# Kernel tuning notes

Measured on AMD Instinct MI355X. Metric: run time of the kernel, lower is better.

The kernel has to match this reference:

```python
import jax, jax.numpy as jnp
import numpy as np

B, T, E, H, L, V = 2, 1024, 1024, 16, 4, 32000
HS = E // H
EPS = 1e-5


def layernorm(x, g, b):
    m = jnp.mean(x, axis=-1, keepdims=True)
    v = jnp.mean((x - m) ** 2, axis=-1, keepdims=True)
    return (x - m) * jax.lax.rsqrt(v + EPS) * g + b


def setup_inputs() -> dict:
    key = jax.random.key(0)
    ks = jax.random.split(key, 20)
    s = 0.02
    inp = {
        "ids": jax.random.randint(ks[0], (B, T), 0, V, dtype=jnp.int32),
        "emb": jax.random.normal(ks[1], (V, E), jnp.float32) * s,
        "pos": jax.random.normal(ks[2], (T, E), jnp.float32) * s,
        "wq": jax.random.normal(ks[3], (L, E, E), jnp.float32) * s,
        "bq": jnp.zeros((L, E), jnp.float32),
        "wk": jax.random.normal(ks[4], (L, E, E), jnp.float32) * s,
        "bk": jnp.zeros((L, E), jnp.float32),
        "wv": jax.random.normal(ks[5], (L, E, E), jnp.float32) * s,
        "bv": jnp.zeros((L, E), jnp.float32),
        "w1": jax.random.normal(ks[6], (L, E, 4 * E), jnp.float32) * s,
        "b1": jnp.zeros((L, 4 * E), jnp.float32),
        "w2": jax.random.normal(ks[7], (L, 4 * E, E), jnp.float32) * s,
        "b2": jnp.zeros((L, E), jnp.float32),
        "ln1_g": jnp.ones((L, E), jnp.float32),
        "ln1_b": jnp.zeros((L, E), jnp.float32),
        "ln2_g": jnp.ones((L, E), jnp.float32),
        "ln2_b": jnp.zeros((L, E), jnp.float32),
        "proj_w": jax.random.normal(ks[8], (E, V), jnp.float32) * s,
        "proj_b": jnp.zeros((V,), jnp.float32),
    }
    return inp


def reference(ids, emb, pos, wq, bq, wk, bk, wv, bv, w1, b1, w2, b2,
              ln1_g, ln1_b, ln2_g, ln2_b, proj_w, proj_b):
    x = emb[ids] + pos[:ids.shape[-1]]  # [B,T,E]
    scale = 1.0 / (E ** 0.5)  # NOTE: original divides by embed_size**0.5
    causal = jnp.tril(jnp.ones((T, T), dtype=bool))
    for l in range(L):
        h = layernorm(x, ln1_g[l], ln1_b[l])
        q = (h @ wq[l] + bq[l]).reshape(B, T, H, HS).transpose(0, 2, 1, 3)
        k = (h @ wk[l] + bk[l]).reshape(B, T, H, HS).transpose(0, 2, 1, 3)
        v = (h @ wv[l] + bv[l]).reshape(B, T, H, HS).transpose(0, 2, 1, 3)
        scores = jnp.einsum('bhqd,bhkd->bhqk', q, k) * scale
        scores = jnp.where(causal, scores, -jnp.inf)
        attn = jax.nn.softmax(scores, axis=-1)
        o = jnp.einsum('bhqk,bhkd->bhqd', attn, v)
        o = o.transpose(0, 2, 1, 3).reshape(B, T, E)
        x = x + o
        h2 = layernorm(x, ln2_g[l], ln2_b[l])
        ff = jax.nn.gelu(h2 @ w1[l] + b1[l], approximate=False) @ w2[l] + b2[l]
        x = x + ff  # Dropout(0.2) in eval mode = identity
    logits = x @ proj_w + proj_b  # [B,T,V]
    return logits
```

## Files before the change

kernel.cpp:

```cpp
#include <hip/hip_runtime.h>
#include <hip/hip_bf16.h>
#include <cstdint>

#define B_    2
#define T_    1024
#define E_    1024
#define H_    16
#define HS_   64
#define L_    4
#define V_    32000
#define FF_   4096
#define BT_   2048
#define EPS_  1e-5f
#define SCALE_ 0.03125f

typedef __bf16 bf16;
typedef bf16  bf16x4 __attribute__((ext_vector_type(4)));
typedef bf16  bf16x8 __attribute__((ext_vector_type(8)));
typedef float f32x4  __attribute__((ext_vector_type(4)));

#define GL2LDS(gp, lp) __builtin_amdgcn_global_load_lds( \
    (const __attribute__((address_space(1))) void*)(gp), \
    (__attribute__((address_space(3))) void*)(lp), 16, 0, 0)

__global__ __launch_bounds__(256) void embed_kernel(
    const int* __restrict__ ids, const float* __restrict__ emb,
    const float* __restrict__ pos, float* __restrict__ x)
{
  int bt = blockIdx.x;
  int t  = bt & (T_ - 1);
  int id = ids[bt];
  f32x4 e = *(const f32x4*)(emb + (size_t)id * E_ + threadIdx.x * 4);
  f32x4 p = *(const f32x4*)(pos + (size_t)t  * E_ + threadIdx.x * 4);
  *(f32x4*)(x + (size_t)bt * E_ + threadIdx.x * 4) = e + p;
}

__device__ __forceinline__ float wred_sum(float v) {
#pragma unroll
  for (int o = 32; o; o >>= 1) v += __shfl_xor(v, o, 64);
  return v;
}

__global__ __launch_bounds__(256) void ln_kernel(
    const float* __restrict__ x, const float* __restrict__ g,
    const float* __restrict__ b, bf16* __restrict__ h)
{
  int row = blockIdx.x, tid = threadIdx.x;
  f32x4 v = *(const f32x4*)(x + (size_t)row * E_ + tid * 4);
  float s  = v[0] + v[1] + v[2] + v[3];
  float sq = v[0]*v[0] + v[1]*v[1] + v[2]*v[2] + v[3]*v[3];
  s  = wred_sum(s);
  sq = wred_sum(sq);
  __shared__ float rs[4], rq[4];
  int w = tid >> 6, lane = tid & 63;
  if (lane == 0) { rs[w] = s; rq[w] = sq; }
  __syncthreads();
  float S = rs[0] + rs[1] + rs[2] + rs[3];
  float Q = rq[0] + rq[1] + rq[2] + rq[3];
  float mean = S * (1.0f / E_);
  float var  = Q * (1.0f / E_) - mean * mean;
  float rstd = rsqrtf(fmaxf(var, 0.0f) + EPS_);
  f32x4 gv = *(const f32x4*)(g + tid * 4);
  f32x4 bv = *(const f32x4*)(b + tid * 4);
  f32x4 o = (v - mean) * rstd * gv + bv;
  bf16x4 ob = { (bf16)o[0], (bf16)o[1], (bf16)o[2], (bf16)o[3] };
  *(bf16x4*)(h + (size_t)row * E_ + tid * 4) = ob;
}

__global__ __launch_bounds__(256) void convw_kernel(
    const float* __restrict__ W0, const float* __restrict__ W1, const float* __restrict__ W2,
    bf16* __restrict__ O0, bf16* __restrict__ O1, bf16* __restrict__ O2,
    int K, int ldW)
{
  int z = blockIdx.z;
  const float* W = (z == 0) ? W0 : (z == 1) ? W1 : W2;
  bf16*        O = (z == 0) ? O0 : (z == 1) ? O1 : O2;
  __shared__ float tl[32][33];
  int n0 = blockIdx.x * 32, k0 = blockIdx.y * 32;
  int c = threadIdx.x & 31, r = threadIdx.x >> 5;
#pragma unroll
  for (int p = 0; p < 4; ++p)
    tl[r + p * 8][c] = W[(size_t)(k0 + r + p * 8) * ldW + n0 + c];
  __syncthreads();
#pragma unroll
  for (int p = 0; p < 4; ++p)
    O[(size_t)(n0 + r + p * 8) * K + k0 + c] = (bf16)tl[c][r + p * 8];
}

template <int ACT, int MODE>
__global__ __launch_bounds__(256) void gemm_bf16(
    const bf16* __restrict__ A,
    const bf16* __restrict__ B0, const bf16* __restrict__ B1, const bf16* __restrict__ B2,
    const float* __restrict__ bi0, const float* __restrict__ bi1, const float* __restrict__ bi2,
    bf16* __restrict__ Cb0, bf16* __restrict__ Cb1, bf16* __restrict__ Cb2,
    float* __restrict__ Cf,
    int K, int ldc, int LDK)
{
  int z = blockIdx.z;
  const bf16*  Bm = (MODE == 3) ? B0 : (z == 0) ? B0 : (z == 1) ? B1 : B2;
  const float* bi = (z == 0) ? bi0 : (z == 1) ? bi1 : bi2;
  bf16*        Cb = (z == 0) ? Cb0 : (z == 1) ? Cb1 : Cb2;
  int koff = (MODE == 3) ? z * K : 0;

  int nb  = (int)(gridDim.x * gridDim.y);
  int lin = blockIdx.x + gridDim.x * blockIdx.y;
  int per = nb >> 3;
  int b   = (lin & 7) * per + (lin >> 3);
  int mi  = b & 15;
  int ni  = b >> 4;

  __shared__ __align__(16) char lds[2][16384];

  int tid = threadIdx.x;
  int lane = tid & 63, wid = tid >> 6;
  int wm = (wid >> 1) * 64, wn = (wid & 1) * 64;
  int fr = lane & 15, fb = lane >> 4;

  const bf16* Asrc = A  + (size_t)(mi * 128) * LDK + koff;
  const bf16* Bsrc = Bm + (size_t)(ni * 128) * LDK + koff;

  int NT = K >> 5;

#define STAGE(buf, kk)                                                          \
  {                                                                             \
    _Pragma("unroll")                                                           \
    for (int is = 0; is < 2; ++is) {                                            \
      int rl = is * 64 + (tid >> 2);                                            \
      int key = (rl >> 1) & 3;                                                  \
      int ck  = ((tid & 3) ^ key) * 8;                                          \
      GL2LDS(Asrc + (size_t)rl * LDK + (kk) + ck,                               \
             lds[buf] + is * 4096 + tid * 16);                                  \
      GL2LDS(Bsrc + (size_t)rl * LDK + (kk) + ck,                               \
             lds[buf] + 8192 + is * 4096 + tid * 16);                           \
    }                                                                           \
  }

  f32x4 acc[4][4];
#pragma unroll
  for (int i = 0; i < 4; ++i)
#pragma unroll
    for (int j = 0; j < 4; ++j) acc[i][j] = (f32x4){0.f, 0.f, 0.f, 0.f};

  STAGE(0, 0);
  int cur = 0;

  for (int t = 0; t < NT; ++t) {
    __syncthreads();
    if (t + 1 < NT) STAGE(cur ^ 1, (t + 1) << 5);

    const char* Ab = lds[cur];
    const char* Bb = lds[cur] + 8192;
    bf16x8 af[4], bfr[4];
#pragma unroll
    for (int i = 0; i < 4; ++i) {
      int rl = wm + i * 16 + fr;
      af[i] = *(const bf16x8*)(Ab + rl * 64 + ((fb ^ ((rl >> 1) & 3)) * 16));
    }
#pragma unroll
    for (int j = 0; j < 4; ++j) {
      int rl = wn + j * 16 + fr;
      bfr[j] = *(const bf16x8*)(Bb + rl * 64 + ((fb ^ ((rl >> 1) & 3)) * 16));
    }
#pragma unroll
    for (int i = 0; i < 4; ++i)
#pragma unroll
      for (int j = 0; j < 4; ++j)
        acc[i][j] = __builtin_amdgcn_mfma_f32_16x16x32_bf16(af[i], bfr[j], acc[i][j], 0, 0, 0);
    cur ^= 1;
  }
#undef STAGE

#pragma unroll
  for (int i = 0; i < 4; ++i) {
#pragma unroll
    for (int j = 0; j < 4; ++j) {
      int gc = ni * 128 + wn + j * 16 + fr;
      float bv = (MODE == 3) ? 0.f : bi[gc];
#pragma unroll
      for (int r = 0; r < 4; ++r) {
        int gr = mi * 128 + wm + i * 16 + fb * 4 + r;
        float vv = acc[i][j][r] + bv;
        if (ACT == 1) vv = 0.5f * vv * (1.0f + erff(vv * 0.70710678118654752f));
        if (MODE == 1) {
          Cb[(size_t)gr * ldc + gc] = (bf16)vv;
        } else {
          Cf[(size_t)(blockIdx.z * BT_ + gr) * ldc + gc] = vv;
        }
      }
    }
  }
}

__global__ __launch_bounds__(256) void combine_kernel(
    const float* __restrict__ p, const float* __restrict__ bi,
    float* __restrict__ x, bf16* __restrict__ xb)
{
  int row = blockIdx.x, tid = threadIdx.x;
  size_t off = (size_t)row * E_ + tid * 4;
  f32x4 a = *(const f32x4*)(p + off);
  f32x4 c = *(const f32x4*)(p + (size_t)BT_ * E_ + off);
  f32x4 bv = *(const f32x4*)(bi + tid * 4);
  f32x4 xv = *(const f32x4*)(x + off);
  f32x4 nv = xv + a + c + bv;
  *(f32x4*)(x + off) = nv;
  bf16x4 ob = { (bf16)nv[0], (bf16)nv[1], (bf16)nv[2], (bf16)nv[3] };
  *(bf16x4*)(xb + off) = ob;
}

__global__ __launch_bounds__(512, 2) void gemm256_kernel(
    const bf16* __restrict__ A, const bf16* __restrict__ Bm,
    const float* __restrict__ bi, float* __restrict__ C, int K, int N)
{
  int nwg = (int)gridDim.x;
  int per = nwg >> 3;
  int bid = (int)blockIdx.x;
  int tl  = (bid & 7) * per + (bid >> 3);
  int mi  = tl & 7, ni = tl >> 3;

  __shared__ __align__(16) char lds[2][65536];

  int tid = threadIdx.x;
  int lane = tid & 63, wid = tid >> 6;
  int wr = wid >> 2, wc = wid & 3;
  int fr = lane & 15, fb = lane >> 4;

  const bf16* Asrc = A  + (size_t)(mi * 256) * K;
  const bf16* Bsrc = Bm + (size_t)(ni * 256) * K;

  int NT = K >> 6;

#define STGQ(buf, kk, h, is)                                               \
  {                                                                        \
    int ri  = (is) * 64 + (tid >> 3);                                      \
    int ck  = (tid & 7) ^ (ri & 7);                                        \
    int row = (h) * 128 + ri;                                              \
    GL2LDS(Asrc + (size_t)row * K + (kk) + ck * 8,                         \
           lds[buf] + (h) * 16384 + (is) * 8192 + tid * 16);               \
    GL2LDS(Bsrc + (size_t)row * K + (kk) + ck * 8,                         \
           lds[buf] + 32768 + (h) * 16384 + (is) * 8192 + tid * 16);       \
  }

  f32x4 acc[8][4];
#pragma unroll
  for (int i = 0; i < 8; ++i)
#pragma unroll
    for (int j = 0; j < 4; ++j) acc[i][j] = (f32x4){0.f, 0.f, 0.f, 0.f};

  STGQ(0, 0, 0, 0); STGQ(0, 0, 0, 1); STGQ(0, 0, 1, 0); STGQ(0, 0, 1, 1);

  for (int t = 0; t < NT; ++t) {
    int buf = t & 1;
    int nk  = (t + 1) << 6;
    bool pf = (t + 1 < NT);

    if (pf) {
      STGQ(buf ^ 1, nk, 0, 0);
      asm volatile("s_waitcnt vmcnt(2)" ::: "memory");
    } else {
      asm volatile("s_waitcnt vmcnt(0)" ::: "memory");
    }
    __builtin_amdgcn_s_barrier();
    asm volatile("" ::: "memory");

    const char* Ab = lds[buf];
    const char* Bb = lds[buf] + 32768;

    bf16x8 bfr[4][2];
#pragma unroll
    for (int n2 = 0; n2 < 4; ++n2) {
      int row = wc * 64 + n2 * 16 + fr;
#pragma unroll
      for (int ks = 0; ks < 2; ++ks)
        bfr[n2][ks] = *(const bf16x8*)(Bb + (row >> 7) * 16384 + (row & 127) * 128
                                          + ((((ks * 4 + fb) ^ (fr & 7))) << 4));
    }

#pragma unroll
    for (int q = 0; q < 4; ++q) {
      bf16x8 af[2][2];
#pragma unroll
      for (int m2 = 0; m2 < 2; ++m2) {
        int ri = (q * 2 + m2) * 16 + fr;
#pragma unroll
        for (int ks = 0; ks < 2; ++ks)
          af[m2][ks] = *(const bf16x8*)(Ab + wr * 16384 + ri * 128
                                           + ((((ks * 4 + fb) ^ (fr & 7))) << 4));
      }
      __builtin_amdgcn_s_setprio(1);
#pragma unroll
      for (int m2 = 0; m2 < 2; ++m2)
#pragma unroll
        for (int n2 = 0; n2 < 4; ++n2)
#pragma unroll
          for (int ks = 0; ks < 2; ++ks)
            acc[q * 2 + m2][n2] = __builtin_amdgcn_mfma_f32_16x16x32_bf16(
                af[m2][ks], bfr[n2][ks], acc[q * 2 + m2][n2], 0, 0, 0);
      __builtin_amdgcn_s_setprio(0);
      if (pf && q == 0) STGQ(buf ^ 1, nk, 0, 1);
      if (pf && q == 1) STGQ(buf ^ 1, nk, 1, 0);
      if (pf && q == 2) STGQ(buf ^ 1, nk, 1, 1);
    }
    asm volatile("" ::: "memory");
    __builtin_amdgcn_s_barrier();
  }
#undef STGQ

#pragma unroll
  for (int i = 0; i < 8; ++i) {
#pragma unroll
    for (int j = 0; j < 4; ++j) {
      int gc = ni * 256 + wc * 64 + j * 16 + fr;
      float bv = bi[gc];
#pragma unroll
      for (int r = 0; r < 4; ++r) {
        int gr = mi * 256 + wr * 128 + i * 16 + fb * 4 + r;
        C[(size_t)gr * N + gc] = acc[i][j][r] + bv;
      }
    }
  }
}

__global__ __launch_bounds__(256) void attn_kernel(
    const bf16* __restrict__ q, const bf16* __restrict__ k,
    const bf16* __restrict__ v, float* __restrict__ x)
{
  __shared__ __align__(16) char Ks[8192];
  __shared__ __align__(16) char Vs[8192];
  __shared__ __align__(16) char Ps[8192];

  int tid = threadIdx.x, lane = tid & 63, w = tid >> 6;
  int qt = blockIdx.x, bh = blockIdx.y;
  int b = bh >> 4, h = bh & 15;
  size_t hoff = (size_t)b * T_ * E_ + h * HS_;
  int fr = lane & 15, fb = lane >> 4;

  bf16x8 qa[2];
  {
    const bf16* qp = q + hoff + (size_t)(qt * 64 + w * 16 + fr) * E_ + fb * 8;
    qa[0] = *(const bf16x8*)qp;
    qa[1] = *(const bf16x8*)(qp + 32);
  }

  f32x4 O[4];
  float m_[4], l_[4];
#pragma unroll
  for (int i = 0; i < 4; ++i) { O[i] = (f32x4){0.f,0.f,0.f,0.f}; m_[i] = -1e30f; l_[i] = 0.f; }

  for (int kt = 0; kt <= qt; ++kt) {
    __syncthreads();
    {
      const bf16* kbase = k + hoff + (size_t)(kt * 64) * E_;
#pragma unroll
      for (int is = 0; is < 2; ++is) {
        int c = is * 32 + (tid >> 3);
        int key = ((c & 7) ^ (c >> 3)) & 7;
        GL2LDS(kbase + (size_t)c * E_ + (((tid & 7) ^ key) * 8),
               Ks + is * 4096 + tid * 16);
      }
    }
#pragma unroll
    for (int p = 0; p < 2; ++p) {
      int row = tid >> 2;
      int d0 = (tid & 3) * 8 + p * 32;
      bf16x8 vv = *(const bf16x8*)(v + hoff + (size_t)(kt * 64 + row) * E_ + d0);
#pragma unroll
      for (int e = 0; e < 8; ++e) {
        int d = d0 + e;
        int key = ((d & 7) ^ (d >> 3)) & 7;
        *(bf16*)(Vs + d * 128 + ((row * 2) ^ (key << 4))) = vv[e];
      }
    }
    __syncthreads();

    f32x4 s[4];
#pragma unroll
    for (int jc = 0; jc < 4; ++jc) {
      s[jc] = (f32x4){0.f, 0.f, 0.f, 0.f};
#pragma unroll
      for (int kc = 0; kc < 2; ++kc) {
        int c = jc * 16 + fr;
        int key = ((c & 7) ^ (c >> 3)) & 7;
        bf16x8 kf = *(const bf16x8*)(Ks + c * 128 + ((kc * 64 + fb * 16) ^ (key << 4)));
        s[jc] = __builtin_amdgcn_mfma_f32_16x16x32_bf16(qa[kc], kf, s[jc], 0, 0, 0);
      }
    }

    char* pbase = Ps + w * 2048;
#pragma unroll
    for (int r = 0; r < 4; ++r) {
      float s0 = s[0][r] * SCALE_, s1 = s[1][r] * SCALE_;
      float s2 = s[2][r] * SCALE_, s3 = s[3][r] * SCALE_;
      int qrow = qt * 64 + w * 16 + fb * 4 + r;
      if (kt == qt) {
        int kc0 = kt * 64 + fr;
        if (kc0      > qrow) s0 = -1e30f;
        if (kc0 + 16 > qrow) s1 = -1e30f;
        if (kc0 + 32 > qrow) s2 = -1e30f;
        if (kc0 + 48 > qrow) s3 = -1e30f;
      }
      float mx = fmaxf(fmaxf(s0, s1), fmaxf(s2, s3));
      mx = fmaxf(mx, __shfl_xor(mx, 1, 16));
      mx = fmaxf(mx, __shfl_xor(mx, 2, 16));
      mx = fmaxf(mx, __shfl_xor(mx, 4, 16));
      mx = fmaxf(mx, __shfl_xor(mx, 8, 16));
      float mnew = fmaxf(m_[r], mx);
      float p0 = __expf(s0 - mnew), p1 = __expf(s1 - mnew);
      float p2 = __expf(s2 - mnew), p3 = __expf(s3 - mnew);
      float rs = p0 + p1 + p2 + p3;
      rs += __shfl_xor(rs, 1, 16);
      rs += __shfl_xor(rs, 2, 16);
      rs += __shfl_xor(rs, 4, 16);
      rs += __shfl_xor(rs, 8, 16);
      float scl = __expf(m_[r] - mnew);
      l_[r] = l_[r] * scl + rs;
      m_[r] = mnew;
#pragma unroll
      for (int jd = 0; jd < 4; ++jd) O[jd][r] *= scl;
      int key2 = (r << 4) ^ (fb << 5);
      char* pr_ = pbase + (fb * 4 + r) * 128;
      *(bf16*)(pr_ + (( 0 + fr * 2) ^ key2)) = (bf16)p0;
      *(bf16*)(pr_ + ((32 + fr * 2) ^ key2)) = (bf16)p1;
      *(bf16*)(pr_ + ((64 + fr * 2) ^ key2)) = (bf16)p2;
      *(bf16*)(pr_ + ((96 + fr * 2) ^ key2)) = (bf16)p3;
    }

#pragma unroll
    for (int kc = 0; kc < 2; ++kc) {
      int key2 = ((fr & 3) << 4) ^ ((fr >> 2) << 5);
      bf16x8 pa = *(const bf16x8*)(pbase + fr * 128 + ((kc * 64 + fb * 16) ^ key2));
#pragma unroll
      for (int jd = 0; jd < 4; ++jd) {
        int d = jd * 16 + fr;
        int key = ((d & 7) ^ (d >> 3)) & 7;
        bf16x8 vf = *(const bf16x8*)(Vs + d * 128 + ((kc * 64 + fb * 16) ^ (key << 4)));
        O[jd] = __builtin_amdgcn_mfma_f32_16x16x32_bf16(pa, vf, O[jd], 0, 0, 0);
      }
    }
  }

#pragma unroll
  for (int r = 0; r < 4; ++r) {
    float inv = 1.0f / l_[r];
    float* xp = x + hoff + (size_t)(qt * 64 + w * 16 + fb * 4 + r) * E_;
#pragma unroll
    for (int jd = 0; jd < 4; ++jd) {
      int d = jd * 16 + fr;
      xp[d] += O[jd][r] * inv;
    }
  }
}

extern "C" void kernel_launch(void* const* d_in, const int* in_sizes, int n_in,
                              void* d_out, int out_size, void* d_ws, size_t ws_size,
                              hipStream_t stream)
{
  const int*   ids  = (const int*)  d_in[0];
  const float* emb  = (const float*)d_in[1];
  const float* pos  = (const float*)d_in[2];
  const float* wq   = (const float*)d_in[3];
  const float* bq   = (const float*)d_in[4];
  const float* wk   = (const float*)d_in[5];
  const float* bk   = (const float*)d_in[6];
  const float* wv   = (const float*)d_in[7];
  const float* bv   = (const float*)d_in[8];
  const float* w1   = (const float*)d_in[9];
  const float* b1   = (const float*)d_in[10];
  const float* w2   = (const float*)d_in[11];
  const float* b2   = (const float*)d_in[12];
  const float* ln1g = (const float*)d_in[13];
  const float* ln1b = (const float*)d_in[14];
  const float* ln2g = (const float*)d_in[15];
  const float* ln2b = (const float*)d_in[16];
  const float* pw   = (const float*)d_in[17];
  const float* pb   = (const float*)d_in[18];
  float* out = (float*)d_out;

  if (ws_size < (size_t)17 * 1024 * 1024 * 4) return;
  float* ws = (float*)d_ws;
  float* x   = ws;
  bf16*  hb  = (bf16*)(ws + (size_t) 2 * 1024 * 1024);
  bf16*  qb  = (bf16*)(ws + (size_t) 3 * 1024 * 1024);
  bf16*  kb  = (bf16*)(ws + (size_t) 4 * 1024 * 1024);
  bf16*  vb  = (bf16*)(ws + (size_t) 5 * 1024 * 1024);
  bf16*  ffb = (bf16*)(ws + (size_t) 6 * 1024 * 1024);
  float* fp  = ws + (size_t)2 * 1024 * 1024;
  bf16*  lwb = (bf16*)(ws + (size_t)10 * 1024 * 1024);
  bf16*  xb  = (bf16*)(ws + (size_t)16 * 1024 * 1024);
  bf16*  pwb = (bf16*)ws;
  bf16*  wqt = lwb;
  bf16*  wkt = lwb + (size_t)1 * 1024 * 1024;
  bf16*  wvt = lwb + (size_t)2 * 1024 * 1024;
  bf16*  w1t = lwb + (size_t)3 * 1024 * 1024;
  bf16*  w2t = lwb + (size_t)7 * 1024 * 1024;

  embed_kernel<<<BT_, 256, 0, stream>>>(ids, emb, pos, x);

  for (int l = 0; l < L_; ++l) {
    const size_t lEE = (size_t)l * E_ * E_;
    const size_t lEF = (size_t)l * E_ * FF_;

    convw_kernel<<<dim3(E_/32, E_/32, 3), 256, 0, stream>>>(
        wq + lEE, wk + lEE, wv + lEE, wqt, wkt, wvt, E_, E_);
    convw_kernel<<<dim3(FF_/32, E_/32, 1), 256, 0, stream>>>(
        w1 + lEF, nullptr, nullptr, w1t, nullptr, nullptr, E_, FF_);
    convw_kernel<<<dim3(E_/32, FF_/32, 1), 256, 0, stream>>>(
        w2 + lEF, nullptr, nullptr, w2t, nullptr, nullptr, FF_, E_);

    ln_kernel<<<BT_, 256, 0, stream>>>(x, ln1g + l*E_, ln1b + l*E_, hb);

    gemm_bf16<0,1><<<dim3(16, E_/128, 3), 256, 0, stream>>>(
        hb, wqt, wkt, wvt, bq + l*E_, bk + l*E_, bv + l*E_,
        qb, kb, vb, nullptr, E_, E_, E_);

    attn_kernel<<<dim3(T_/64, B_*H_), 256, 0, stream>>>(qb, kb, vb, x);

    ln_kernel<<<BT_, 256, 0, stream>>>(x, ln2g + l*E_, ln2b + l*E_, hb);

    gemm_bf16<1,1><<<dim3(16, FF_/128, 1), 256, 0, stream>>>(
        hb, w1t, nullptr, nullptr, b1 + (size_t)l*FF_, nullptr, nullptr,
        ffb, nullptr, nullptr, nullptr, E_, FF_, E_);

    gemm_bf16<0,3><<<dim3(16, E_/128, 2), 256, 0, stream>>>(
        ffb, w2t, nullptr, nullptr, nullptr, nullptr, nullptr,
        nullptr, nullptr, nullptr, fp, FF_/2, E_, FF_);
    combine_kernel<<<BT_, 256, 0, stream>>>(fp, b2 + l*E_, x, xb);
  }

  convw_kernel<<<dim3(V_/32, E_/32, 1), 256, 0, stream>>>(
      pw, nullptr, nullptr, pwb, nullptr, nullptr, E_, V_);
  gemm256_kernel<<<(V_/256) * 8, 512, 0, stream>>>(
      xb, pwb, pb, out, E_, V_);
}
```

Before: 852.8 us.

## Deepen LM-head GEMM prefetch pipeline and fuse residual combine with next LayerNorm

The 256x256 projection GEMM now splits A and B staging, prefetching B two K-tiles ahead into the current buffer and A one tile ahead, with a barrier per quarter-step so global-to-LDS loads overlap MFMA work more evenly. Separately, the FF2 split-K combine is fused with the next layer's LN1, so one ln_kernel launch and one read of x are dropped per layer for layers 1-3. The fused LayerNorm uses a single-pass sum and sum-of-squares variance, which is less numerically robust than the two-pass form. The extra barriers in the GEMM loop add synchronisation cost.

```diff
diff --git a/kernel.cpp b/kernel.cpp
--- a/kernel.cpp
+++ b/kernel.cpp
@@ -207,6 +207,40 @@
   *(bf16x4*)(xb + off) = ob;
 }
 
+__global__ __launch_bounds__(256) void combine_ln_kernel(
+    const float* __restrict__ p, const float* __restrict__ bi,
+    const float* __restrict__ g, const float* __restrict__ b,
+    float* __restrict__ x, bf16* __restrict__ h)
+{
+  int row = blockIdx.x, tid = threadIdx.x;
+  size_t off = (size_t)row * E_ + tid * 4;
+  f32x4 a = *(const f32x4*)(p + off);
+  f32x4 c = *(const f32x4*)(p + (size_t)BT_ * E_ + off);
+  f32x4 bv = *(const f32x4*)(bi + tid * 4);
+  f32x4 xv = *(const f32x4*)(x + off);
+  f32x4 nv = xv + a + c + bv;
+  *(f32x4*)(x + off) = nv;
+
+  float s  = nv[0] + nv[1] + nv[2] + nv[3];
+  float sq = nv[0]*nv[0] + nv[1]*nv[1] + nv[2]*nv[2] + nv[3]*nv[3];
+  s  = wred_sum(s);
+  sq = wred_sum(sq);
+  __shared__ float rs[4], rq[4];
+  int w = tid >> 6, lane = tid & 63;
+  if (lane == 0) { rs[w] = s; rq[w] = sq; }
+  __syncthreads();
+  float S = rs[0] + rs[1] + rs[2] + rs[3];
+  float Q = rq[0] + rq[1] + rq[2] + rq[3];
+  float mean = S * (1.0f / E_);
+  float var  = Q * (1.0f / E_) - mean * mean;
+  float rstd = rsqrtf(fmaxf(var, 0.0f) + EPS_);
+  f32x4 gv = *(const f32x4*)(g + tid * 4);
+  f32x4 bbv = *(const f32x4*)(b + tid * 4);
+  f32x4 o = (nv - mean) * rstd * gv + bbv;
+  bf16x4 ob = { (bf16)o[0], (bf16)o[1], (bf16)o[2], (bf16)o[3] };
+  *(bf16x4*)(h + off) = ob;
+}
+
 __global__ __launch_bounds__(512, 2) void gemm256_kernel(
     const bf16* __restrict__ A, const bf16* __restrict__ Bm,
     const float* __restrict__ bi, float* __restrict__ C, int K, int N)
@@ -229,16 +263,24 @@
 
   int NT = K >> 6;
 
-#define STGQ(buf, kk, h, is)                                               \
-  {                                                                        \
-    int ri  = (is) * 64 + (tid >> 3);                                      \
-    int ck  = (tid & 7) ^ (ri & 7);                                        \
-    int row = (h) * 128 + ri;                                              \
-    GL2LDS(Asrc + (size_t)row * K + (kk) + ck * 8,                         \
-           lds[buf] + (h) * 16384 + (is) * 8192 + tid * 16);               \
-    GL2LDS(Bsrc + (size_t)row * K + (kk) + ck * 8,                         \
-           lds[buf] + 32768 + (h) * 16384 + (is) * 8192 + tid * 16);       \
-  }
+#define STG_A(buf, kk, h)                                                  \
+  { _Pragma("unroll")                                                      \
+    for (int is = 0; is < 2; ++is) {                                       \
+      int ri  = is * 64 + (tid >> 3);                                      \
+      int ck  = (tid & 7) ^ (ri & 7);                                      \
+      int row = (h) * 128 + ri;                                            \
+      GL2LDS(Asrc + (size_t)row * K + (kk) + ck * 8,                       \
+             lds[buf] + (h) * 16384 + is * 8192 + tid * 16);               \
+    } }
+#define STG_B(buf, kk, h)                                                  \
+  { _Pragma("unroll")                                                      \
+    for (int is = 0; is < 2; ++is) {                                       \
+      int ri  = is * 64 + (tid >> 3);                                      \
+      int ck  = (tid & 7) ^ (ri & 7);                                      \
+      int row = (h) * 128 + ri;                                            \
+      GL2LDS(Bsrc + (size_t)row * K + (kk) + ck * 8,                       \
+             lds[buf] + 32768 + (h) * 16384 + is * 8192 + tid * 16);       \
+    } }
 
   f32x4 acc[8][4];
 #pragma unroll
@@ -246,37 +288,36 @@
 #pragma unroll
     for (int j = 0; j < 4; ++j) acc[i][j] = (f32x4){0.f, 0.f, 0.f, 0.f};
 
-  STGQ(0, 0, 0, 0); STGQ(0, 0, 0, 1); STGQ(0, 0, 1, 0); STGQ(0, 0, 1, 1);
+  STG_B(0, 0, 0); STG_B(0, 0, 1); STG_A(0, 0, 0); STG_A(0, 0, 1);
+  if (NT > 1) {
+    STG_B(1, 64, 0); STG_B(1, 64, 1);
+    asm volatile("s_waitcnt vmcnt(4)" ::: "memory");
+  } else {
+    asm volatile("s_waitcnt vmcnt(0)" ::: "memory");
+  }
+  __builtin_amdgcn_s_barrier();
 
   for (int t = 0; t < NT; ++t) {
     int buf = t & 1;
-    int nk  = (t + 1) << 6;
-    bool pf = (t + 1 < NT);
-
-    if (pf) {
-      STGQ(buf ^ 1, nk, 0, 0);
-      asm volatile("s_waitcnt vmcnt(2)" ::: "memory");
-    } else {
-      asm volatile("s_waitcnt vmcnt(0)" ::: "memory");
-    }
-    __builtin_amdgcn_s_barrier();
-    asm volatile("" ::: "memory");
+    int k1 = (t + 1) << 6, k2 = (t + 2) << 6;
+    bool p1 = (t + 1 < NT), p2 = (t + 2 < NT);
 
     const char* Ab = lds[buf];
     const char* Bb = lds[buf] + 32768;
 
     bf16x8 bfr[4][2];
 #pragma unroll
-    for (int n2 = 0; n2 < 4; ++n2) {
-      int row = wc * 64 + n2 * 16 + fr;
-#pragma unroll
-      for (int ks = 0; ks < 2; ++ks)
-        bfr[n2][ks] = *(const bf16x8*)(Bb + (row >> 7) * 16384 + (row & 127) * 128
-                                          + ((((ks * 4 + fb) ^ (fr & 7))) << 4));
-    }
-
-#pragma unroll
     for (int q = 0; q < 4; ++q) {
+      if (q == 0) {
+#pragma unroll
+        for (int n2 = 0; n2 < 4; ++n2) {
+          int row = wc * 64 + n2 * 16 + fr;
+#pragma unroll
+          for (int ks = 0; ks < 2; ++ks)
+            bfr[n2][ks] = *(const bf16x8*)(Bb + (row >> 7) * 16384 + (row & 127) * 128
+                                              + ((((ks * 4 + fb) ^ (fr & 7))) << 4));
+        }
+      }
       bf16x8 af[2][2];
 #pragma unroll
       for (int m2 = 0; m2 < 2; ++m2) {
@@ -286,6 +327,17 @@
           af[m2][ks] = *(const bf16x8*)(Ab + wr * 16384 + ri * 128
                                            + ((((ks * 4 + fb) ^ (fr & 7))) << 4));
       }
+      if (q == 0 && p1) STG_A(buf ^ 1, k1, 0);
+      if (q == 1 && p1) STG_A(buf ^ 1, k1, 1);
+      if (q == 2 && p2) STG_B(buf, k2, 0);
+      if (q == 3 && p2) STG_B(buf, k2, 1);
+      if (q == 3 && p1) {
+        if (p2) asm volatile("s_waitcnt vmcnt(4)" ::: "memory");
+        else    asm volatile("s_waitcnt vmcnt(0)" ::: "memory");
+      }
+      __builtin_amdgcn_s_barrier();
+      asm volatile("s_waitcnt lgkmcnt(0)" ::: "memory");
+      __builtin_amdgcn_sched_barrier(0);
       __builtin_amdgcn_s_setprio(1);
 #pragma unroll
       for (int m2 = 0; m2 < 2; ++m2)
@@ -296,14 +348,11 @@
             acc[q * 2 + m2][n2] = __builtin_amdgcn_mfma_f32_16x16x32_bf16(
                 af[m2][ks], bfr[n2][ks], acc[q * 2 + m2][n2], 0, 0, 0);
       __builtin_amdgcn_s_setprio(0);
-      if (pf && q == 0) STGQ(buf ^ 1, nk, 0, 1);
-      if (pf && q == 1) STGQ(buf ^ 1, nk, 1, 0);
-      if (pf && q == 2) STGQ(buf ^ 1, nk, 1, 1);
-    }
-    asm volatile("" ::: "memory");
-    __builtin_amdgcn_s_barrier();
-  }
-#undef STGQ
+      __builtin_amdgcn_s_barrier();
+    }
+  }
+#undef STG_A
+#undef STG_B
 
 #pragma unroll
   for (int i = 0; i < 8; ++i) {
@@ -485,6 +534,7 @@
   bf16*  ffb = (bf16*)(ws + (size_t) 6 * 1024 * 1024);
   float* fp  = ws + (size_t)2 * 1024 * 1024;
   bf16*  lwb = (bf16*)(ws + (size_t)10 * 1024 * 1024);
+  bf16*  hb2 = (bf16*)(ws + (size_t)15 * 1024 * 1024 + 512 * 1024);
   bf16*  xb  = (bf16*)(ws + (size_t)16 * 1024 * 1024);
   bf16*  pwb = (bf16*)ws;
   bf16*  wqt = lwb;
@@ -494,10 +544,12 @@
   bf16*  w2t = lwb + (size_t)7 * 1024 * 1024;
 
   embed_kernel<<<BT_, 256, 0, stream>>>(ids, emb, pos, x);
+  ln_kernel<<<BT_, 256, 0, stream>>>(x, ln1g, ln1b, hb);
 
   for (int l = 0; l < L_; ++l) {
     const size_t lEE = (size_t)l * E_ * E_;
     const size_t lEF = (size_t)l * E_ * FF_;
+    const bf16* hcur = (l == 0) ? hb : hb2;
 
     convw_kernel<<<dim3(E_/32, E_/32, 3), 256, 0, stream>>>(
         wq + lEE, wk + lEE, wv + lEE, wqt, wkt, wvt, E_, E_);
@@ -506,10 +558,8 @@
     convw_kernel<<<dim3(E_/32, FF_/32, 1), 256, 0, stream>>>(
         w2 + lEF, nullptr, nullptr, w2t, nullptr, nullptr, FF_, E_);
 
-    ln_kernel<<<BT_, 256, 0, stream>>>(x, ln1g + l*E_, ln1b + l*E_, hb);
-
     gemm_bf16<0,1><<<dim3(16, E_/128, 3), 256, 0, stream>>>(
-        hb, wqt, wkt, wvt, bq + l*E_, bk + l*E_, bv + l*E_,
+        hcur, wqt, wkt, wvt, bq + l*E_, bk + l*E_, bv + l*E_,
         qb, kb, vb, nullptr, E_, E_, E_);
 
     attn_kernel<<<dim3(T_/64, B_*H_), 256, 0, stream>>>(qb, kb, vb, x);
@@ -523,7 +573,12 @@
     gemm_bf16<0,3><<<dim3(16, E_/128, 2), 256, 0, stream>>>(
         ffb, w2t, nullptr, nullptr, nullptr, nullptr, nullptr,
         nullptr, nullptr, nullptr, fp, FF_/2, E_, FF_);
-    combine_kernel<<<BT_, 256, 0, stream>>>(fp, b2 + l*E_, x, xb);
+    if (l < L_ - 1) {
+      combine_ln_kernel<<<BT_, 256, 0, stream>>>(
+          fp, b2 + l*E_, ln1g + (l+1)*E_, ln1b + (l+1)*E_, x, hb2);
+    } else {
+      combine_kernel<<<BT_, 256, 0, stream>>>(fp, b2 + l*E_, x, xb);
+    }
   }
 
   convw_kernel<<<dim3(V_/32, E_/32, 1), 256, 0, stream>>>(
```

Measured after the change: 839.7 us. About the same (-1.5%).

## Fuse layernorm into embed and combine kernels, reverse attention tile order

Applied to the files above, without the earlier changes.

Fuses the first-layer layernorm into the embedding kernel and the next layer's ln1 into the residual combine kernel, removing one launch and one full read of x per layer. A separate hb2 buffer holds the layernorm output so later writes to the shared workspace don't clobber it. Attention blocks are now scheduled in reverse query-tile order so the longest causal tiles start first, improving load balance. The hb2 placement must not overlap live buffers such as the fp partials or the lwb weights.

```diff
diff --git a/kernel.cpp b/kernel.cpp
--- a/kernel.cpp
+++ b/kernel.cpp
@@ -23,30 +23,15 @@
     (const __attribute__((address_space(1))) void*)(gp), \
     (__attribute__((address_space(3))) void*)(lp), 16, 0, 0)
 
-__global__ __launch_bounds__(256) void embed_kernel(
-    const int* __restrict__ ids, const float* __restrict__ emb,
-    const float* __restrict__ pos, float* __restrict__ x)
-{
-  int bt = blockIdx.x;
-  int t  = bt & (T_ - 1);
-  int id = ids[bt];
-  f32x4 e = *(const f32x4*)(emb + (size_t)id * E_ + threadIdx.x * 4);
-  f32x4 p = *(const f32x4*)(pos + (size_t)t  * E_ + threadIdx.x * 4);
-  *(f32x4*)(x + (size_t)bt * E_ + threadIdx.x * 4) = e + p;
-}
-
 __device__ __forceinline__ float wred_sum(float v) {
 #pragma unroll
   for (int o = 32; o; o >>= 1) v += __shfl_xor(v, o, 64);
   return v;
 }
 
-__global__ __launch_bounds__(256) void ln_kernel(
-    const float* __restrict__ x, const float* __restrict__ g,
-    const float* __restrict__ b, bf16* __restrict__ h)
-{
-  int row = blockIdx.x, tid = threadIdx.x;
-  f32x4 v = *(const f32x4*)(x + (size_t)row * E_ + tid * 4);
+__device__ __forceinline__ void ln_body(
+    f32x4 v, const float* g, const float* b, bf16* h, size_t off, int tid)
+{
   float s  = v[0] + v[1] + v[2] + v[3];
   float sq = v[0]*v[0] + v[1]*v[1] + v[2]*v[2] + v[3]*v[3];
   s  = wred_sum(s);
@@ -64,7 +49,33 @@
   f32x4 bv = *(const f32x4*)(b + tid * 4);
   f32x4 o = (v - mean) * rstd * gv + bv;
   bf16x4 ob = { (bf16)o[0], (bf16)o[1], (bf16)o[2], (bf16)o[3] };
-  *(bf16x4*)(h + (size_t)row * E_ + tid * 4) = ob;
+  *(bf16x4*)(h + off) = ob;
+}
+
+__global__ __launch_bounds__(256) void embed_ln_kernel(
+    const int* __restrict__ ids, const float* __restrict__ emb,
+    const float* __restrict__ pos, const float* __restrict__ g,
+    const float* __restrict__ b, float* __restrict__ x, bf16* __restrict__ h)
+{
+  int bt = blockIdx.x, tid = threadIdx.x;
+  int t  = bt & (T_ - 1);
+  int id = ids[bt];
+  f32x4 e = *(const f32x4*)(emb + (size_t)id * E_ + tid * 4);
+  f32x4 p = *(const f32x4*)(pos + (size_t)t  * E_ + tid * 4);
+  f32x4 v = e + p;
+  size_t off = (size_t)bt * E_ + tid * 4;
+  *(f32x4*)(x + off) = v;
+  ln_body(v, g, b, h, off, tid);
+}
+
+__global__ __launch_bounds__(256) void ln_kernel(
+    const float* __restrict__ x, const float* __restrict__ g,
+    const float* __restrict__ b, bf16* __restrict__ h)
+{
+  int row = blockIdx.x, tid = threadIdx.x;
+  size_t off = (size_t)row * E_ + tid * 4;
+  f32x4 v = *(const f32x4*)(x + off);
+  ln_body(v, g, b, h, off, tid);
 }
 
 __global__ __launch_bounds__(256) void convw_kernel(
@@ -207,6 +218,22 @@
   *(bf16x4*)(xb + off) = ob;
 }
 
+__global__ __launch_bounds__(256) void combine_ln_kernel(
+    const float* __restrict__ p, const float* __restrict__ bi,
+    const float* __restrict__ g, const float* __restrict__ b,
+    float* __restrict__ x, bf16* __restrict__ h)
+{
+  int row = blockIdx.x, tid = threadIdx.x;
+  size_t off = (size_t)row * E_ + tid * 4;
+  f32x4 a = *(const f32x4*)(p + off);
+  f32x4 c = *(const f32x4*)(p + (size_t)BT_ * E_ + off);
+  f32x4 bv = *(const f32x4*)(bi + tid * 4);
+  f32x4 xv = *(const f32x4*)(x + off);
+  f32x4 nv = xv + a + c + bv;
+  *(f32x4*)(x + off) = nv;
+  ln_body(nv, g, b, h, off, tid);
+}
+
 __global__ __launch_bounds__(512, 2) void gemm256_kernel(
     const bf16* __restrict__ A, const bf16* __restrict__ Bm,
     const float* __restrict__ bi, float* __restrict__ C, int K, int N)
@@ -329,7 +356,8 @@
   __shared__ __align__(16) char Ps[8192];
 
   int tid = threadIdx.x, lane = tid & 63, w = tid >> 6;
-  int qt = blockIdx.x, bh = blockIdx.y;
+  int qt = (int)gridDim.x - 1 - (int)blockIdx.x;
+  int bh = blockIdx.y;
   int b = bh >> 4, h = bh & 15;
   size_t hoff = (size_t)b * T_ * E_ + h * HS_;
   int fr = lane & 15, fb = lane >> 4;
@@ -485,6 +513,7 @@
   bf16*  ffb = (bf16*)(ws + (size_t) 6 * 1024 * 1024);
   float* fp  = ws + (size_t)2 * 1024 * 1024;
   bf16*  lwb = (bf16*)(ws + (size_t)10 * 1024 * 1024);
+  bf16*  hb2 = (bf16*)(ws + (size_t)15 * 1024 * 1024 + 512 * 1024);
   bf16*  xb  = (bf16*)(ws + (size_t)16 * 1024 * 1024);
   bf16*  pwb = (bf16*)ws;
   bf16*  wqt = lwb;
@@ -493,11 +522,12 @@
   bf16*  w1t = lwb + (size_t)3 * 1024 * 1024;
   bf16*  w2t = lwb + (size_t)7 * 1024 * 1024;
 
-  embed_kernel<<<BT_, 256, 0, stream>>>(ids, emb, pos, x);
+  embed_ln_kernel<<<BT_, 256, 0, stream>>>(ids, emb, pos, ln1g, ln1b, x, hb);
 
   for (int l = 0; l < L_; ++l) {
     const size_t lEE = (size_t)l * E_ * E_;
     const size_t lEF = (size_t)l * E_ * FF_;
+    const bf16* hcur = (l == 0) ? hb : hb2;
 
     convw_kernel<<<dim3(E_/32, E_/32, 3), 256, 0, stream>>>(
         wq + lEE, wk + lEE, wv + lEE, wqt, wkt, wvt, E_, E_);
@@ -506,10 +536,8 @@
     convw_kernel<<<dim3(E_/32, FF_/32, 1), 256, 0, stream>>>(
         w2 + lEF, nullptr, nullptr, w2t, nullptr, nullptr, FF_, E_);
 
-    ln_kernel<<<BT_, 256, 0, stream>>>(x, ln1g + l*E_, ln1b + l*E_, hb);
-
     gemm_bf16<0,1><<<dim3(16, E_/128, 3), 256, 0, stream>>>(
-        hb, wqt, wkt, wvt, bq + l*E_, bk + l*E_, bv + l*E_,
+        hcur, wqt, wkt, wvt, bq + l*E_, bk + l*E_, bv + l*E_,
         qb, kb, vb, nullptr, E_, E_, E_);
 
     attn_kernel<<<dim3(T_/64, B_*H_), 256, 0, stream>>>(qb, kb, vb, x);
@@ -523,7 +551,12 @@
     gemm_bf16<0,3><<<dim3(16, E_/128, 2), 256, 0, stream>>>(
         ffb, w2t, nullptr, nullptr, nullptr, nullptr, nullptr,
         nullptr, nullptr, nullptr, fp, FF_/2, E_, FF_);
-    combine_kernel<<<BT_, 256, 0, stream>>>(fp, b2 + l*E_, x, xb);
+    if (l < L_ - 1) {
+      combine_ln_kernel<<<BT_, 256, 0, stream>>>(
+          fp, b2 + l*E_, ln1g + (l+1)*E_, ln1b + (l+1)*E_, x, hb2);
+    } else {
+      combine_kernel<<<BT_, 256, 0, stream>>>(fp, b2 + l*E_, x, xb);
+    }
   }
 
   convw_kernel<<<dim3(V_/32, E_/32, 1), 256, 0, stream>>>(
```

New measurement: 830.3 us. 2.6% less time.
